# Kernel tuning notes

Hardware: AMD Instinct MI355X
Metric: run time of the kernel (lower is better)

Reference implementation:

```python
import jax, jax.numpy as jnp
import numpy as np

K = 9
VOCAB = 7
DIM = 512
LOW = 256  # downsampled bottleneck dim
N_LAYERS = 2
EPS = 1e-5


def _inorm(x, g, b):
    # InstanceNorm1d over length axis (biased var), x: (N, C, K)
    m = jnp.mean(x, axis=-1, keepdims=True)
    v = jnp.mean((x - m) ** 2, axis=-1, keepdims=True)
    return g[None, :, None] * (x - m) * jax.lax.rsqrt(v + EPS) + b[None, :, None]


def _conv5_same(x, w, b):
    # x: (N, C, K), w: (O, C, 5), dilation 1, padding 'same' -> pad 2
    y = jax.lax.conv_general_dilated(
        x, w, window_strides=(1,), padding=[(2, 2)],
        dimension_numbers=('NCH', 'OIH', 'NCH'))
    return y + b[None, :, None]


def _bytenet_layer(x, p):
    (g1, b1, g2, b2, g3, b3, w1, c1b, w2, c2b, w3, c3b) = p
    h = jax.nn.gelu(_inorm(x, g1, b1), approximate=False)
    h = jnp.einsum('nck,oc->nok', h, w1) + c1b[None, :, None]      # 1x1 conv 512->256
    h = jax.nn.gelu(_inorm(h, g2, b2), approximate=False)
    h = _conv5_same(h, w2, c2b)                                     # k=5 conv 256->256
    h = jax.nn.gelu(_inorm(h, g3, b3), approximate=False)
    h = jnp.einsum('nck,oc->nok', h, w3) + c3b[None, :, None]      # 1x1 conv 256->512
    return h + x  # dropout is identity in eval


def setup_inputs() -> dict:
    key = jax.random.key(0)
    ks = jax.random.split(key, 16)
    x = jax.random.randint(ks[0], (8, 2048), 0, VOCAB)
    emb = jax.random.normal(ks[1], (VOCAB, DIM), jnp.float32) * 0.02
    emb = emb.at[6].set(0.0)  # padding_idx=6
    d = {
        'x': x,
        'emb': emb,
        'ln1_w': jnp.ones((N_LAYERS, DIM)), 'ln1_b': jnp.zeros((N_LAYERS, DIM)),
        'ln2_w': jnp.ones((N_LAYERS, LOW)), 'ln2_b': jnp.zeros((N_LAYERS, LOW)),
        'ln3_w': jnp.ones((N_LAYERS, LOW)), 'ln3_b': jnp.zeros((N_LAYERS, LOW)),
        'c1_w': jax.random.normal(ks[2], (N_LAYERS, LOW, DIM), jnp.float32) * 0.02,
        'c1_b': jnp.zeros((N_LAYERS, LOW)),
        'c2_w': jax.random.normal(ks[3], (N_LAYERS, LOW, LOW, 5), jnp.float32) * 0.02,
        'c2_b': jnp.zeros((N_LAYERS, LOW)),
        'c3_w': jax.random.normal(ks[4], (N_LAYERS, DIM, LOW), jnp.float32) * 0.02,
        'c3_b': jnp.zeros((N_LAYERS, DIM)),
        'out_w': jax.random.normal(ks[5], (VOCAB, DIM * K), jnp.float32) * 0.02,
        'out_b': jnp.zeros((VOCAB,)),
    }
    return d


def reference(x, emb, ln1_w, ln1_b, ln2_w, ln2_b, ln3_w, ln3_b,
              c1_w, c1_b, c2_w, c2_b, c3_w, c3_b, out_w, out_b):
    B, L = x.shape
    W = L - K + 1
    e = emb[x]                                        # (B, L, D)
    idx = jnp.arange(W)[:, None] + jnp.arange(K)      # (W, K)
    win = e[:, idx, :]                                # (B, W, K, D)
    h = win.transpose(0, 1, 3, 2).reshape(B * W, DIM, K)  # (N, D, K)
    for i in range(N_LAYERS):
        p = (ln1_w[i], ln1_b[i], ln2_w[i], ln2_b[i], ln3_w[i], ln3_b[i],
             c1_w[i], c1_b[i], c2_w[i], c2_b[i], c3_w[i], c3_b[i])
        h = _bytenet_layer(h, p)
    pred = h.reshape(B * W, DIM * K) @ out_w.T + out_b
    return pred.reshape(B, W, VOCAB)
```

## Files before the change

### kernel.cpp

```cpp
#include <hip/hip_runtime.h>

typedef __attribute__((ext_vector_type(8))) short bfv8;
typedef __attribute__((ext_vector_type(4))) float f32x4;
typedef __attribute__((ext_vector_type(4))) unsigned short usv4;

typedef __attribute__((address_space(1))) const void gvoid;
typedef __attribute__((address_space(3))) void lvoid;
__device__ __forceinline__ void gload16(const void* g, void* l) {
  __builtin_amdgcn_global_load_lds((gvoid*)g, (lvoid*)l, 16, 0, 0);
}

__device__ __forceinline__ float bf2f(unsigned short u) {
  union { unsigned int i; float f; } c; c.i = ((unsigned int)u) << 16; return c.f;
}
__device__ __forceinline__ unsigned short f2bf(float f) {
  union { float f; unsigned int i; } c; c.f = f;
  unsigned int r = c.i + 0x7FFFu + ((c.i >> 16) & 1u);
  return (unsigned short)(r >> 16);
}
__device__ __forceinline__ float gelu_(float x) {
  float z2 = 1.5957691216057308f * x * __builtin_fmaf(0.044715f, x * x, 1.0f);
  float e = __expf(z2);
  float t = __builtin_amdgcn_rcpf(e + 1.0f);
  return x - x * t;
}
__device__ __forceinline__ int div9(int col) {
  return (int)(__umulhi((unsigned)col, 954437177u) >> 1);
}

#define CHP 132

__global__ void k_prep(const float* c1w, const float* c2w, const float* c3w,
                       const float* outw, unsigned short* W1b, unsigned short* W2t,
                       unsigned short* W3b, float* OWt) {
  int i = blockIdx.x * 256 + threadIdx.x;
  if (i < 262144) { W1b[i] = f2bf(c1w[i]); return; }
  i -= 262144;
  if (i < 655360) {
    int ii = i & 255, o = (i >> 8) & 255, rest = i >> 16;
    int t = rest % 5, l = rest / 5;
    W2t[i] = f2bf(c2w[(((l * 256 + o) << 8) + ii) * 5 + t]);
    return;
  }
  i -= 655360;
  if (i < 262144) { W3b[i] = f2bf(c3w[i]); return; }
  i -= 262144;
  if (i < 32256) {
    int c = i & 511, rk = i >> 9;
    int r = rk / 9, k = rk - 9 * r;
    OWt[i] = outw[r * 4608 + c * 9 + k];
  }
}

__global__ void k_xng(const int* x, const float* emb, const float* g,
                      const float* bb, unsigned short* X, unsigned short* T,
                      int n0) {
  int idx = blockIdx.x * 256 + threadIdx.x;
  int c = idx & 511, nl = idx >> 9;
  int gn = n0 + nl, b = gn >> 11, w = gn & 2047;
  size_t rbase = (size_t)(12 + nl * 12) * 512 + c;
  float v[9], s = 0.f;
  for (int k = 0; k < 9; k++) {
    int t = w + k; if (t > 2047) t = 2047;
    v[k] = emb[x[(b << 11) + t] * 512 + c];
    X[rbase + k * 512] = f2bf(v[k]);
    s += v[k];
  }
  float m = s * (1.0f / 9.0f), q = 0.f;
  for (int k = 0; k < 9; k++) { float d = v[k] - m; q += d * d; }
  float r = rsqrtf(q * (1.0f / 9.0f) + 1e-5f);
  float gg = g[c], bo = bb[c];
  for (int k = 0; k < 9; k++)
    T[rbase + k * 512] = f2bf(gelu_(gg * (v[k] - m) * r + bo));
}

__global__ void k_zpad(unsigned short* AL) {
  int i = threadIdx.x;
  for (; i < 12 * 256; i += 256) AL[i] = 0;
}

template <int MODE, bool WT>
__global__ __launch_bounds__(512) void k_gemm(
    const unsigned short* __restrict__ Aw, const unsigned short* __restrict__ Bsrc,
    const float* __restrict__ cbias, const float* __restrict__ gw,
    const float* __restrict__ gb, unsigned short* __restrict__ Out,
    unsigned short* __restrict__ Tout) {
  __shared__ __align__(16) char smem[51200];
  unsigned short* lA = (unsigned short*)smem;
  unsigned short* lB = (unsigned short*)(smem + 32768);
  unsigned short* sE = (unsigned short*)smem;

  const int KROW = (MODE == 0) ? 512 : 256;
  int tid = threadIdx.x, wv = tid >> 6, ln = tid & 63;
  int lr = ln >> 3, lu = ln & 7;
  int m0 = (MODE == 2) ? (blockIdx.y << 8) : 0;
  int w0 = blockIdx.x << 4;
  int col0 = blockIdx.x * 144;

  int brow[3], bsw[3];
  #pragma unroll
  for (int s = 0; s < 3; s++) {
    int winst = (s < 2) ? (s * 8 + wv) : (16 + wv);
    int cl = winst * 8 + lr;
    int colg = col0 + cl;
    brow[s] = colg + 3 * div9(colg) + 12;
    bsw[s] = (lu ^ (cl & 7)) << 3;
  }
  int arow = (wv << 3) + lr;

  f32x4 acc[2][9];
  #pragma unroll
  for (int i = 0; i < 2; i++)
    #pragma unroll
    for (int j = 0; j < 9; j++) acc[i][j] = (f32x4){0.f, 0.f, 0.f, 0.f};

  int ksteps = (MODE == 1) ? 20 : (KROW >> 6);
  for (int ks = 0; ks < ksteps; ks++) {
    int kb, dlt; const unsigned short* Ab;
    if (MODE == 1) {
      int t = ks >> 2; kb = (ks & 3) << 6; dlt = t - 2; Ab = Aw + t * 65536;
    } else { kb = ks << 6; dlt = 0; Ab = Aw; }

    #pragma unroll
    for (int p = 0; p < 4; p++) {
      int m = (p << 6) + arow;
      gload16(Ab + (size_t)(m0 + m) * KROW + kb + ((lu ^ (m & 7)) << 3),
              lA + ((p << 6) + (wv << 3)) * 64);
    }
    #pragma unroll
    for (int s = 0; s < 2; s++)
      gload16(Bsrc + (size_t)(brow[s] + dlt) * KROW + kb + bsw[s],
              lB + ((s << 3) + wv) * 512);
    if (wv < 2)
      gload16(Bsrc + (size_t)(brow[2] + dlt) * KROW + kb + bsw[2],
              lB + (16 + wv) * 512);
    __syncthreads();

    int l16 = ln & 15, loct = ln >> 4;
    #pragma unroll
    for (int kk = 0; kk < 2; kk++) {
      int kbyte = (kk << 6) + (loct << 4);
      bfv8 af[2], bf_[9];
      #pragma unroll
      for (int mi = 0; mi < 2; mi++) {
        int row = (wv << 5) + (mi << 4) + l16;
        af[mi] = *(const bfv8*)((const char*)lA + row * 128 + (kbyte ^ ((row & 7) << 4)));
      }
      #pragma unroll
      for (int ni = 0; ni < 9; ni++) {
        int row = (ni << 4) + l16;
        bf_[ni] = *(const bfv8*)((const char*)lB + row * 128 + (kbyte ^ ((row & 7) << 4)));
      }
      #pragma unroll
      for (int mi = 0; mi < 2; mi++)
        #pragma unroll
        for (int ni = 0; ni < 9; ni++)
          acc[mi][ni] = __builtin_amdgcn_mfma_f32_16x16x32_bf16(
              af[mi], bf_[ni], acc[mi][ni], 0, 0, 0);
    }
    __syncthreads();
  }

  int l16 = ln & 15, loct = ln >> 4;
  int c4 = tid & 31, win = tid >> 5;
  #pragma unroll
  for (int R = 0; R < 2; R++) {
    if (R) __syncthreads();
    if ((wv >> 2) == R) {
      #pragma unroll
      for (int mi = 0; mi < 2; mi++) {
        int chh = ((wv & 3) << 5) + (mi << 4) + (loct << 2);
        #pragma unroll
        for (int ni = 0; ni < 9; ni++) {
          int col = (ni << 4) + l16;
          usv4 pk;
          #pragma unroll
          for (int q = 0; q < 4; q++) pk[q] = f2bf(acc[mi][ni][q]);
          *(usv4*)(sE + col * CHP + chh) = pk;
        }
      }
    }
    __syncthreads();

    int chl = (R << 7) + (c4 << 2);
    const unsigned short* sb = sE + (win * 9) * CHP + (c4 << 2);
    float s1[4] = {0.f, 0.f, 0.f, 0.f}, s2[4] = {0.f, 0.f, 0.f, 0.f};
    float v[9][4];
    size_t ob;
    if (MODE == 2) {
      int chg = m0 + chl;
      ob = (size_t)(12 + (w0 + win) * 12) * 512 + chg;
      float cb[4];
      #pragma unroll
      for (int j = 0; j < 4; j++) cb[j] = cbias[chg + j];
      #pragma unroll
      for (int k = 0; k < 9; k++) {
        usv4 rv = *(const usv4*)(sb + k * CHP);
        usv4 old = *(usv4*)(Out + ob + k * 512);
        usv4 pk;
        #pragma unroll
        for (int j = 0; j < 4; j++) {
          float f = bf2f(rv[j]) + cb[j] + bf2f(old[j]);
          v[k][j] = f; s1[j] += f; s2[j] = __builtin_fmaf(f, f, s2[j]);
          pk[j] = f2bf(f);
        }
        *(usv4*)(Out + ob + k * 512) = pk;
      }
    } else {
      ob = (size_t)(12 + (w0 + win) * 12) * 256 + chl;
      #pragma unroll
      for (int k = 0; k < 9; k++) {
        usv4 rv = *(const usv4*)(sb + k * CHP);
        #pragma unroll
        for (int j = 0; j < 4; j++) {
          float f = bf2f(rv[j]);
          s1[j] += f; s2[j] = __builtin_fmaf(f, f, s2[j]);
        }
      }
    }
    if (MODE != 2 || WT) {
      float mn[4], rr[4], gg[4], bo[4];
      int gi = (MODE == 2) ? (m0 + chl) : chl;
      #pragma unroll
      for (int j = 0; j < 4; j++) {
        mn[j] = s1[j] * (1.0f / 9.0f);
        float var = s2[j] * (1.0f / 9.0f) - mn[j] * mn[j];
        rr[j] = rsqrtf(var + 1e-5f);
        gg[j] = gw[gi + j]; bo[j] = gb[gi + j];
      }
      #pragma unroll
      for (int k = 0; k < 9; k++) {
        usv4 pk;
        if (MODE == 2) {
          #pragma unroll
          for (int j = 0; j < 4; j++)
            pk[j] = f2bf(gelu_(gg[j] * (v[k][j] - mn[j]) * rr[j] + bo[j]));
          *(usv4*)(Tout + ob + k * 512) = pk;
        } else {
          usv4 rv = *(const usv4*)(sb + k * CHP);
          #pragma unroll
          for (int j = 0; j < 4; j++)
            pk[j] = f2bf(gelu_(gg[j] * (bf2f(rv[j]) - mn[j]) * rr[j] + bo[j]));
          *(usv4*)(Out + ob + k * 256) = pk;
        }
      }
      if (MODE == 0) {
        usv4 z = (usv4){0, 0, 0, 0};
        *(usv4*)(Out + ob + 9 * 256) = z;
        *(usv4*)(Out + ob + 10 * 256) = z;
        *(usv4*)(Out + ob + 11 * 256) = z;
      }
    }
  }
}

__global__ void k_out(const unsigned short* X, const float* OWt, const float* outb,
                      float* pred, int n0, int nc) {
  int gw = (blockIdx.x * 256 + threadIdx.x) >> 6;
  int ln = threadIdx.x & 63;
  if (gw >= nc) return;
  int gn = n0 + gw, b = gn >> 11, w = gn & 2047;
  if (w >= 2040) return;
  const unsigned short* xb = X + (size_t)(12 + gw * 12) * 512 + ln * 8;
  float a[7];
  #pragma unroll
  for (int r = 0; r < 7; r++) a[r] = 0.f;
  for (int k = 0; k < 9; k++) {
    bfv8 xv = *(const bfv8*)(xb + k * 512);
    float xf[8];
    #pragma unroll
    for (int j = 0; j < 8; j++) xf[j] = bf2f((unsigned short)xv[j]);
    #pragma unroll
    for (int r = 0; r < 7; r++) {
      const float* wp = OWt + (r * 9 + k) * 512 + ln * 8;
      float4 w0 = *(const float4*)(wp);
      float4 w1 = *(const float4*)(wp + 4);
      a[r] += xf[0] * w0.x + xf[1] * w0.y + xf[2] * w0.z + xf[3] * w0.w +
              xf[4] * w1.x + xf[5] * w1.y + xf[6] * w1.z + xf[7] * w1.w;
    }
  }
  #pragma unroll
  for (int r = 0; r < 7; r++)
    for (int off = 32; off; off >>= 1) a[r] += __shfl_down(a[r], off);
  if (ln == 0) {
    float* o = pred + (size_t)(b * 2040 + w) * 7;
    #pragma unroll
    for (int r = 0; r < 7; r++) o[r] = a[r] + outb[r];
  }
}

extern "C" void kernel_launch(void* const* d_in, const int* in_sizes, int n_in,
                              void* d_out, int out_size, void* d_ws, size_t ws_size,
                              hipStream_t stream) {
  const int*   x    = (const int*)d_in[0];
  const float* emb  = (const float*)d_in[1];
  const float* ln1w = (const float*)d_in[2];
  const float* ln1b = (const float*)d_in[3];
  const float* ln2w = (const float*)d_in[4];
  const float* ln2b = (const float*)d_in[5];
  const float* ln3w = (const float*)d_in[6];
  const float* ln3b = (const float*)d_in[7];
  const float* c1w  = (const float*)d_in[8];
  const float* c2w  = (const float*)d_in[10];
  const float* c3w  = (const float*)d_in[12];
  const float* c3b  = (const float*)d_in[13];
  const float* outw = (const float*)d_in[14];
  const float* outb = (const float*)d_in[15];
  float* pred = (float*)d_out;

  int nc = 16384;
  while (nc > 128 &&
         2488320ull + (unsigned long long)(nc + 1) * 36864ull > ws_size)
    nc >>= 1;
  int tiles = nc >> 4;
  int nchunks = 16384 / nc;

  char* ws = (char*)d_ws;
  unsigned short* W1b = (unsigned short*)(ws);
  unsigned short* W2t = (unsigned short*)(ws + 524288);
  unsigned short* W3b = (unsigned short*)(ws + 1835008);
  float*          OWt = (float*)(ws + 2359296);
  char* act = ws + 2488320;
  size_t hiB = (size_t)(nc + 1) * 12288;
  size_t loB = (size_t)(nc + 1) * 6144;
  unsigned short* X   = (unsigned short*)(act);
  unsigned short* T   = (unsigned short*)(act + hiB);
  unsigned short* AL  = (unsigned short*)(act + 2 * hiB);
  unsigned short* AL2 = (unsigned short*)(act + 2 * hiB + loB);

  k_prep<<<(1211904 + 255) / 256, 256, 0, stream>>>(c1w, c2w, c3w, outw,
                                                    W1b, W2t, W3b, OWt);

  for (int ch = 0; ch < nchunks; ch++) {
    int n0 = ch * nc;
    k_zpad<<<1, 256, 0, stream>>>(AL);
    k_xng<<<nc * 2, 256, 0, stream>>>(x, emb, ln1w, ln1b, X, T, n0);
    for (int l = 0; l < 2; l++) {
      k_gemm<0, false><<<dim3(tiles, 1), 512, 0, stream>>>(
          W1b + l * 131072, T, nullptr, ln2w + l * 256, ln2b + l * 256,
          AL, nullptr);
      k_gemm<1, false><<<dim3(tiles, 1), 512, 0, stream>>>(
          W2t + l * 327680, AL, nullptr, ln3w + l * 256, ln3b + l * 256,
          AL2, nullptr);
      if (l == 0)
        k_gemm<2, true><<<dim3(tiles, 2), 512, 0, stream>>>(
            W3b + l * 131072, AL2, c3b + l * 512, ln1w + 512, ln1b + 512,
            X, T);
      else
        k_gemm<2, false><<<dim3(tiles, 2), 512, 0, stream>>>(
            W3b + l * 131072, AL2, c3b + l * 512, nullptr, nullptr,
            X, nullptr);
    }
    k_out<<<nc / 4, 256, 0, stream>>>(X, OWt, outb, pred, n0, nc);
  }
}
```

Baseline: 862.6 us.

## Fuse first InstanceNorm+GELU into GEMM prologue and halve column tile

Drops the separate normalized T buffer. The layer-input InstanceNorm+GELU is now computed in LDS inside the first GEMM after loading the raw X tile, and the residual GEMM no longer writes a normalized copy. The column tile per block shrinks from 16 windows (144 columns) to 8 windows (72 columns), with fewer accumulators, lower LDS use and a launch-bounds occupancy hint. This removes a full activation write and read per layer and raises occupancy. In exchange, weight tiles are reused across fewer columns, the MODE 0 k-loop gains an extra barrier, and part of each block idles during the epilogue.

```diff
diff --git a/kernel.cpp b/kernel.cpp
--- a/kernel.cpp
+++ b/kernel.cpp
@@ -52,26 +52,15 @@
   }
 }
 
-__global__ void k_xng(const int* x, const float* emb, const float* g,
-                      const float* bb, unsigned short* X, unsigned short* T,
-                      int n0) {
+__global__ void k_x0(const int* x, const float* emb, unsigned short* X, int n0) {
   int idx = blockIdx.x * 256 + threadIdx.x;
   int c = idx & 511, nl = idx >> 9;
   int gn = n0 + nl, b = gn >> 11, w = gn & 2047;
-  size_t rbase = (size_t)(12 + nl * 12) * 512 + c;
-  float v[9], s = 0.f;
+  unsigned short* dst = X + (size_t)(12 + nl * 12) * 512 + c;
   for (int k = 0; k < 9; k++) {
     int t = w + k; if (t > 2047) t = 2047;
-    v[k] = emb[x[(b << 11) + t] * 512 + c];
-    X[rbase + k * 512] = f2bf(v[k]);
-    s += v[k];
-  }
-  float m = s * (1.0f / 9.0f), q = 0.f;
-  for (int k = 0; k < 9; k++) { float d = v[k] - m; q += d * d; }
-  float r = rsqrtf(q * (1.0f / 9.0f) + 1e-5f);
-  float gg = g[c], bo = bb[c];
-  for (int k = 0; k < 9; k++)
-    T[rbase + k * 512] = f2bf(gelu_(gg * (v[k] - m) * r + bo));
+    dst[k * 512] = f2bf(emb[x[(b << 11) + t] * 512 + c]);
+  }
 }
 
 __global__ void k_zpad(unsigned short* AL) {
@@ -79,13 +68,13 @@
   for (; i < 12 * 256; i += 256) AL[i] = 0;
 }
 
-template <int MODE, bool WT>
-__global__ __launch_bounds__(512) void k_gemm(
+template <int MODE>
+__global__ __launch_bounds__(512, 4) void k_gemm(
     const unsigned short* __restrict__ Aw, const unsigned short* __restrict__ Bsrc,
-    const float* __restrict__ cbias, const float* __restrict__ gw,
-    const float* __restrict__ gb, unsigned short* __restrict__ Out,
-    unsigned short* __restrict__ Tout) {
-  __shared__ __align__(16) char smem[51200];
+    const float* __restrict__ cbias, const float* __restrict__ n1w,
+    const float* __restrict__ n1b, const float* __restrict__ gw,
+    const float* __restrict__ gb, unsigned short* __restrict__ Out, int nkc) {
+  __shared__ __align__(16) char smem[43008];
   unsigned short* lA = (unsigned short*)smem;
   unsigned short* lB = (unsigned short*)(smem + 32768);
   unsigned short* sE = (unsigned short*)smem;
@@ -94,25 +83,24 @@
   int tid = threadIdx.x, wv = tid >> 6, ln = tid & 63;
   int lr = ln >> 3, lu = ln & 7;
   int m0 = (MODE == 2) ? (blockIdx.y << 8) : 0;
-  int w0 = blockIdx.x << 4;
-  int col0 = blockIdx.x * 144;
-
-  int brow[3], bsw[3];
-  #pragma unroll
-  for (int s = 0; s < 3; s++) {
-    int winst = (s < 2) ? (s * 8 + wv) : (16 + wv);
-    int cl = winst * 8 + lr;
-    int colg = col0 + cl;
-    brow[s] = colg + 3 * div9(colg) + 12;
-    bsw[s] = (lu ^ (cl & 7)) << 3;
-  }
+  int w0 = blockIdx.x << 3;
+  int col0 = blockIdx.x * 72;
+
+  int cl0 = (wv << 3) + lr;
+  int colg0 = col0 + cl0; if (colg0 >= nkc) colg0 = nkc - 1;
+  int brow0 = colg0 + 3 * div9(colg0) + 12;
+  int bsw0 = (lu ^ (cl0 & 7)) << 3;
+  int cl1 = 64 + (wv << 3) + lr;
+  int colg1 = col0 + cl1; if (colg1 >= nkc) colg1 = nkc - 1;
+  int brow1 = colg1 + 3 * div9(colg1) + 12;
+  int bsw1 = (lu ^ (cl1 & 7)) << 3;
   int arow = (wv << 3) + lr;
 
-  f32x4 acc[2][9];
+  f32x4 acc[2][5];
   #pragma unroll
   for (int i = 0; i < 2; i++)
     #pragma unroll
-    for (int j = 0; j < 9; j++) acc[i][j] = (f32x4){0.f, 0.f, 0.f, 0.f};
+    for (int j = 0; j < 5; j++) acc[i][j] = (f32x4){0.f, 0.f, 0.f, 0.f};
 
   int ksteps = (MODE == 1) ? 20 : (KROW >> 6);
   for (int ks = 0; ks < ksteps; ks++) {
@@ -127,34 +115,55 @@
       gload16(Ab + (size_t)(m0 + m) * KROW + kb + ((lu ^ (m & 7)) << 3),
               lA + ((p << 6) + (wv << 3)) * 64);
     }
-    #pragma unroll
-    for (int s = 0; s < 2; s++)
-      gload16(Bsrc + (size_t)(brow[s] + dlt) * KROW + kb + bsw[s],
-              lB + ((s << 3) + wv) * 512);
+    gload16(Bsrc + (size_t)(brow0 + dlt) * KROW + kb + bsw0,
+            lB + ((wv << 3)) * 64);
     if (wv < 2)
-      gload16(Bsrc + (size_t)(brow[2] + dlt) * KROW + kb + bsw[2],
-              lB + (16 + wv) * 512);
+      gload16(Bsrc + (size_t)(brow1 + dlt) * KROW + kb + bsw1,
+              lB + ((64 + (wv << 3))) * 64);
     __syncthreads();
+
+    if (MODE == 0) {
+      int gch = kb + ln;
+      float gg = n1w[gch], bo = n1b[gch];
+      float v[9], s = 0.f;
+      #pragma unroll
+      for (int k = 0; k < 9; k++) {
+        int cl = wv * 9 + k;
+        v[k] = bf2f(lB[cl * 64 + (((ln >> 3) ^ (cl & 7)) << 3) + (ln & 7)]);
+        s += v[k];
+      }
+      float mn = s * (1.0f / 9.0f), q = 0.f;
+      #pragma unroll
+      for (int k = 0; k < 9; k++) { float d = v[k] - mn; q += d * d; }
+      float r = rsqrtf(q * (1.0f / 9.0f) + 1e-5f);
+      #pragma unroll
+      for (int k = 0; k < 9; k++) {
+        int cl = wv * 9 + k;
+        lB[cl * 64 + (((ln >> 3) ^ (cl & 7)) << 3) + (ln & 7)] =
+            f2bf(gelu_(gg * (v[k] - mn) * r + bo));
+      }
+      __syncthreads();
+    }
 
     int l16 = ln & 15, loct = ln >> 4;
     #pragma unroll
     for (int kk = 0; kk < 2; kk++) {
       int kbyte = (kk << 6) + (loct << 4);
-      bfv8 af[2], bf_[9];
+      bfv8 af[2], bf_[5];
       #pragma unroll
       for (int mi = 0; mi < 2; mi++) {
         int row = (wv << 5) + (mi << 4) + l16;
         af[mi] = *(const bfv8*)((const char*)lA + row * 128 + (kbyte ^ ((row & 7) << 4)));
       }
       #pragma unroll
-      for (int ni = 0; ni < 9; ni++) {
+      for (int ni = 0; ni < 5; ni++) {
         int row = (ni << 4) + l16;
         bf_[ni] = *(const bfv8*)((const char*)lB + row * 128 + (kbyte ^ ((row & 7) << 4)));
       }
       #pragma unroll
       for (int mi = 0; mi < 2; mi++)
         #pragma unroll
-        for (int ni = 0; ni < 9; ni++)
+        for (int ni = 0; ni < 5; ni++)
           acc[mi][ni] = __builtin_amdgcn_mfma_f32_16x16x32_bf16(
               af[mi], bf_[ni], acc[mi][ni], 0, 0, 0);
     }
@@ -171,7 +180,7 @@
       for (int mi = 0; mi < 2; mi++) {
         int chh = ((wv & 3) << 5) + (mi << 4) + (loct << 2);
         #pragma unroll
-        for (int ni = 0; ni < 9; ni++) {
+        for (int ni = 0; ni < 5; ni++) {
           int col = (ni << 4) + l16;
           usv4 pk;
           #pragma unroll
@@ -181,74 +190,60 @@
       }
     }
     __syncthreads();
-
-    int chl = (R << 7) + (c4 << 2);
-    const unsigned short* sb = sE + (win * 9) * CHP + (c4 << 2);
-    float s1[4] = {0.f, 0.f, 0.f, 0.f}, s2[4] = {0.f, 0.f, 0.f, 0.f};
-    float v[9][4];
-    size_t ob;
-    if (MODE == 2) {
-      int chg = m0 + chl;
-      ob = (size_t)(12 + (w0 + win) * 12) * 512 + chg;
-      float cb[4];
-      #pragma unroll
-      for (int j = 0; j < 4; j++) cb[j] = cbias[chg + j];
-      #pragma unroll
-      for (int k = 0; k < 9; k++) {
-        usv4 rv = *(const usv4*)(sb + k * CHP);
-        usv4 old = *(usv4*)(Out + ob + k * 512);
-        usv4 pk;
-        #pragma unroll
-        for (int j = 0; j < 4; j++) {
-          float f = bf2f(rv[j]) + cb[j] + bf2f(old[j]);
-          v[k][j] = f; s1[j] += f; s2[j] = __builtin_fmaf(f, f, s2[j]);
-          pk[j] = f2bf(f);
-        }
-        *(usv4*)(Out + ob + k * 512) = pk;
-      }
-    } else {
-      ob = (size_t)(12 + (w0 + win) * 12) * 256 + chl;
-      #pragma unroll
-      for (int k = 0; k < 9; k++) {
-        usv4 rv = *(const usv4*)(sb + k * CHP);
-        #pragma unroll
-        for (int j = 0; j < 4; j++) {
-          float f = bf2f(rv[j]);
-          s1[j] += f; s2[j] = __builtin_fmaf(f, f, s2[j]);
-        }
-      }
-    }
-    if (MODE != 2 || WT) {
-      float mn[4], rr[4], gg[4], bo[4];
-      int gi = (MODE == 2) ? (m0 + chl) : chl;
-      #pragma unroll
-      for (int j = 0; j < 4; j++) {
-        mn[j] = s1[j] * (1.0f / 9.0f);
-        float var = s2[j] * (1.0f / 9.0f) - mn[j] * mn[j];
-        rr[j] = rsqrtf(var + 1e-5f);
-        gg[j] = gw[gi + j]; bo[j] = gb[gi + j];
-      }
-      #pragma unroll
-      for (int k = 0; k < 9; k++) {
-        usv4 pk;
-        if (MODE == 2) {
+    if (tid < 256) {
+      int chl = (R << 7) + (c4 << 2);
+      const unsigned short* sb = sE + (win * 9) * CHP + (c4 << 2);
+      if (MODE == 2) {
+        int chg = m0 + chl;
+        size_t ob = (size_t)(12 + (size_t)(w0 + win) * 12) * 512 + chg;
+        float cb[4];
+        #pragma unroll
+        for (int j = 0; j < 4; j++) cb[j] = cbias[chg + j];
+        #pragma unroll
+        for (int k = 0; k < 9; k++) {
+          usv4 rv = *(const usv4*)(sb + k * CHP);
+          usv4 old = *(usv4*)(Out + ob + k * 512);
+          usv4 pk;
           #pragma unroll
           for (int j = 0; j < 4; j++)
-            pk[j] = f2bf(gelu_(gg[j] * (v[k][j] - mn[j]) * rr[j] + bo[j]));
-          *(usv4*)(Tout + ob + k * 512) = pk;
-        } else {
+            pk[j] = f2bf(bf2f(rv[j]) + cb[j] + bf2f(old[j]));
+          *(usv4*)(Out + ob + k * 512) = pk;
+        }
+      } else {
+        size_t ob = (size_t)(12 + (size_t)(w0 + win) * 12) * 256 + chl;
+        float s1[4] = {0.f, 0.f, 0.f, 0.f}, s2[4] = {0.f, 0.f, 0.f, 0.f};
+        #pragma unroll
+        for (int k = 0; k < 9; k++) {
           usv4 rv = *(const usv4*)(sb + k * CHP);
+          #pragma unroll
+          for (int j = 0; j < 4; j++) {
+            float f = bf2f(rv[j]);
+            s1[j] += f; s2[j] = __builtin_fmaf(f, f, s2[j]);
+          }
+        }
+        float mn[4], rr[4], gg[4], bo[4];
+        #pragma unroll
+        for (int j = 0; j < 4; j++) {
+          mn[j] = s1[j] * (1.0f / 9.0f);
+          float var = s2[j] * (1.0f / 9.0f) - mn[j] * mn[j];
+          rr[j] = rsqrtf(var + 1e-5f);
+          gg[j] = gw[chl + j]; bo[j] = gb[chl + j];
+        }
+        #pragma unroll
+        for (int k = 0; k < 9; k++) {
+          usv4 rv = *(const usv4*)(sb + k * CHP);
+          usv4 pk;
           #pragma unroll
           for (int j = 0; j < 4; j++)
             pk[j] = f2bf(gelu_(gg[j] * (bf2f(rv[j]) - mn[j]) * rr[j] + bo[j]));
           *(usv4*)(Out + ob + k * 256) = pk;
         }
-      }
-      if (MODE == 0) {
-        usv4 z = (usv4){0, 0, 0, 0};
-        *(usv4*)(Out + ob + 9 * 256) = z;
-        *(usv4*)(Out + ob + 10 * 256) = z;
-        *(usv4*)(Out + ob + 11 * 256) = z;
+        if (MODE == 0) {
+          usv4 z = (usv4){0, 0, 0, 0};
+          *(usv4*)(Out + ob + 9 * 256) = z;
+          *(usv4*)(Out + ob + 10 * 256) = z;
+          *(usv4*)(Out + ob + 11 * 256) = z;
+        }
       }
     }
   }
@@ -310,9 +305,10 @@
 
   int nc = 16384;
   while (nc > 128 &&
-         2488320ull + (unsigned long long)(nc + 1) * 36864ull > ws_size)
+         2488320ull + (unsigned long long)(nc + 1) * 24576ull > ws_size)
     nc >>= 1;
-  int tiles = nc >> 4;
+  int nkc = nc * 9;
+  int tiles = nc >> 3;
   int nchunks = 16384 / nc;
 
   char* ws = (char*)d_ws;
@@ -324,32 +320,26 @@
   size_t hiB = (size_t)(nc + 1) * 12288;
   size_t loB = (size_t)(nc + 1) * 6144;
   unsigned short* X   = (unsigned short*)(act);
-  unsigned short* T   = (unsigned short*)(act + hiB);
-  unsigned short* AL  = (unsigned short*)(act + 2 * hiB);
-  unsigned short* AL2 = (unsigned short*)(act + 2 * hiB + loB);
+  unsigned short* AL  = (unsigned short*)(act + hiB);
+  unsigned short* AL2 = (unsigned short*)(act + hiB + loB);
 
   k_prep<<<(1211904 + 255) / 256, 256, 0, stream>>>(c1w, c2w, c3w, outw,
                                                     W1b, W2t, W3b, OWt);
+  k_zpad<<<1, 256, 0, stream>>>(AL);
 
   for (int ch = 0; ch < nchunks; ch++) {
     int n0 = ch * nc;
-    k_zpad<<<1, 256, 0, stream>>>(AL);
-    k_xng<<<nc * 2, 256, 0, stream>>>(x, emb, ln1w, ln1b, X, T, n0);
+    k_x0<<<nc * 2, 256, 0, stream>>>(x, emb, X, n0);
     for (int l = 0; l < 2; l++) {
-      k_gemm<0, false><<<dim3(tiles, 1), 512, 0, stream>>>(
-          W1b + l * 131072, T, nullptr, ln2w + l * 256, ln2b + l * 256,
-          AL, nullptr);
-      k_gemm<1, false><<<dim3(tiles, 1), 512, 0, stream>>>(
-          W2t + l * 327680, AL, nullptr, ln3w + l * 256, ln3b + l * 256,
-          AL2, nullptr);
-      if (l == 0)
-        k_gemm<2, true><<<dim3(tiles, 2), 512, 0, stream>>>(
-            W3b + l * 131072, AL2, c3b + l * 512, ln1w + 512, ln1b + 512,
-            X, T);
-      else
-        k_gemm<2, false><<<dim3(tiles, 2), 512, 0, stream>>>(
-            W3b + l * 131072, AL2, c3b + l * 512, nullptr, nullptr,
-            X, nullptr);
+      k_gemm<0><<<dim3(tiles, 1), 512, 0, stream>>>(
+          W1b + l * 131072, X, nullptr, ln1w + l * 512, ln1b + l * 512,
+          ln2w + l * 256, ln2b + l * 256, AL, nkc);
+      k_gemm<1><<<dim3(tiles, 1), 512, 0, stream>>>(
+          W2t + l * 327680, AL, nullptr, nullptr, nullptr,
+          ln3w + l * 256, ln3b + l * 256, AL2, nkc);
+      k_gemm<2><<<dim3(tiles, 2), 512, 0, stream>>>(
+          W3b + l * 131072, AL2, c3b + l * 512, nullptr, nullptr,
+          nullptr, nullptr, X, nkc);
     }
     k_out<<<nc / 4, 256, 0, stream>>>(X, OWt, outb, pred, n0, nc);
   }
```

After: 844.4 us. 1.02x faster.
